# Optimization experiments

Hardware: AMD Instinct MI355X
Metric: run time of the kernel (lower is better)

Reference implementation:

```python
import jax, jax.numpy as jnp
import numpy as np

N_NODES = 50000
N_EDGES = 800000
N_FEAT = 256
HIDDEN = 128
N_CLASSES = 40


def gcn_conv(x, src, dst, W, b, n_nodes):
    """PyG GCNConv: add self-loops, symmetric normalization, x@W then scatter-add."""
    h = x @ W  # [N, out]
    loop = jnp.arange(n_nodes, dtype=src.dtype)
    s = jnp.concatenate([src, loop])  # [E+N]
    d = jnp.concatenate([dst, loop])
    deg = jax.ops.segment_sum(jnp.ones_like(d, dtype=h.dtype), d, num_segments=n_nodes)
    dinv = jnp.where(deg > 0, jax.lax.rsqrt(deg), 0.0)
    norm = dinv[s] * dinv[d]  # [E+N]
    msg = h[s] * norm[:, None]  # gather + scale
    out = jax.ops.segment_sum(msg, d, num_segments=n_nodes)  # scatter-add to targets
    return out + b


def setup_inputs() -> dict:
    key = jax.random.key(0)
    k1, k2, k3, k4 = jax.random.split(key, 4)
    x = jax.random.normal(k1, (N_NODES, N_FEAT), dtype=jnp.float32)
    edge_index = jax.random.randint(k2, (2, N_EDGES), 0, N_NODES, dtype=jnp.int32)
    # Glorot-style init for conv weights, zero bias (PyG default)
    W1 = jax.random.normal(k3, (N_FEAT, HIDDEN), dtype=jnp.float32) * (1.0 / np.sqrt(N_FEAT))
    b1 = jnp.zeros((HIDDEN,), dtype=jnp.float32)
    W2 = jax.random.normal(k4, (HIDDEN, N_CLASSES), dtype=jnp.float32) * (1.0 / np.sqrt(HIDDEN))
    b2 = jnp.zeros((N_CLASSES,), dtype=jnp.float32)
    return {"x": x, "edge_index": edge_index, "W1": W1, "b1": b1, "W2": W2, "b2": b2}


def reference(x, edge_index, W1, b1, W2, b2):
    # eval mode: dropout is identity
    src, dst = edge_index[0], edge_index[1]
    h = gcn_conv(x, src, dst, W1, b1, N_NODES)
    h = jax.nn.relu(h)
    h = gcn_conv(h, src, dst, W2, b2, N_NODES)
    return jax.nn.log_softmax(h, axis=1)
```

## Files before the change

kernel.cpp:

```cpp
#include <hip/hip_runtime.h>
#include <hip/hip_fp16.h>
#include <cstdint>

#define N_NODES 50000
#define N_EDGES 800000
#define N_FEAT 256
#define HIDDEN 128
#define N_CLASSES 40
#define NBUCKET 196
#define EPB 3125
#define BCAP 8192
#define ROWS_PAD 50048
#define G1_BLOCKS 782
#define H2S 64

typedef _Float16 half8 __attribute__((ext_vector_type(8)));
typedef __fp16 fp16x2 __attribute__((ext_vector_type(2)));
typedef __attribute__((ext_vector_type(4))) float f32x4;

__device__ inline ushort f2h(float f) {
    return __half_as_ushort(__float2half_rn(f));
}
__device__ inline __half2 u2h2(uint u) {
    union { uint u; __half2 h; } v; v.u = u; return v.h;
}
__device__ inline uint h22u(__half2 h) {
    union { __half2 h; uint u; } v; v.h = h; return v.u;
}


__global__ __launch_bounds__(256) void partition_repack(
        const int* __restrict__ src, const int* __restrict__ dst,
        int* __restrict__ cursor, uint* __restrict__ ebuf,
        const float* __restrict__ W1, ushort* __restrict__ Bp1,
        const float* __restrict__ W2, ushort* __restrict__ Bp2) {
    __shared__ int h[NBUCKET];
    __shared__ int base[NBUCKET];
    __shared__ int cur[NBUCKET];
    int blk = blockIdx.x, t = threadIdx.x;
    int gid = blk * 256 + t;
    if (gid < 32768) {
        int j = gid & 7, lane = (gid >> 3) & 63, kt = (gid >> 9) & 7, nt = gid >> 12;
        int k = kt * 32 + (lane >> 4) * 8 + j;
        int n = nt * 16 + (lane & 15);
        Bp1[gid] = f2h(W1[k * HIDDEN + n]);
    } else if (gid < 32768 + 6144) {
        int i2 = gid - 32768;
        int j = i2 & 7, lane = (i2 >> 3) & 63, kt = (i2 >> 9) & 3, nt = i2 >> 11;
        int k = kt * 32 + (lane >> 4) * 8 + j;
        int n = nt * 16 + (lane & 15);
        Bp2[i2] = (n < N_CLASSES) ? f2h(W2[k * N_CLASSES + n]) : (ushort)0;
    }
    if (t < NBUCKET) { h[t] = 0; cur[t] = 0; }
    __syncthreads();
    int eb = blk * EPB;
    for (int i = t; i < EPB; i += 256)
        atomicAdd(&h[dst[eb + i] >> 8], 1);
    __syncthreads();
    if (t < NBUCKET)
        base[t] = (h[t] > 0) ? atomicAdd(&cursor[t], h[t]) : 0;
    __syncthreads();
    for (int i = t; i < EPB; i += 256) {
        int d = dst[eb + i], sv = src[eb + i];
        int bk = d >> 8;
        int p = base[bk] + atomicAdd(&cur[bk], 1);
        ebuf[bk * BCAP + p] = ((uint)d << 16) | (uint)sv;
    }
}


__global__ __launch_bounds__(256) void csr_gemm1(
        const uint* __restrict__ ebuf, const int* __restrict__ cursor,
        int* __restrict__ deg, float* __restrict__ dinv,
        int* __restrict__ rowptr, int* __restrict__ esrc,
        const float* __restrict__ x, const ushort* __restrict__ Bp,
        ushort* __restrict__ h1h) {
    if (blockIdx.x < NBUCKET) {
        __shared__ int s[256];
        __shared__ int cnt[256];
        __shared__ int exc[256];
        __shared__ int cur[256];
        int b = blockIdx.x, t = threadIdx.x;
        s[t] = (t < NBUCKET) ? cursor[t] : 0;
        __syncthreads();
        for (int off = 1; off < 256; off <<= 1) {
            int t2 = 0;
            if (t >= off) t2 = s[t - off];
            __syncthreads();
            s[t] += t2;
            __syncthreads();
        }
        int beg = (b > 0) ? s[b - 1] : 0;
        int ecnt = s[b] - beg;
        __syncthreads();
        cnt[t] = 0;
        cur[t] = 0;
        __syncthreads();
        const uint* eb = ebuf + (size_t)b * BCAP;
        for (int i = t; i < ecnt; i += 256)
            atomicAdd(&cnt[(eb[i] >> 16) & 255], 1);
        __syncthreads();
        int d = cnt[t];
        s[t] = d;
        __syncthreads();
        for (int off = 1; off < 256; off <<= 1) {
            int t2 = 0;
            if (t >= off) t2 = s[t - off];
            __syncthreads();
            s[t] += t2;
            __syncthreads();
        }
        exc[t] = s[t] - d;
        int node = b * 256 + t;
        if (node < N_NODES) {
            deg[node] = d;
            dinv[node] = rsqrtf((float)(d + 1));
            rowptr[node] = beg + exc[t];
        }
        __syncthreads();
        for (int i = t; i < ecnt; i += 256) {
            uint u = eb[i];
            int dl = (int)(u >> 16) & 255;
            int pos = beg + exc[dl] + atomicAdd(&cur[dl], 1);
            esrc[pos] = (int)(u & 0xffffu);
        }
    } else {
        int t = threadIdx.x;
        int lane = t & 63, w = t >> 6;
        int r = lane & 15, q = lane >> 4;
        int row0 = (blockIdx.x - NBUCKET) * 64;
        int arow = row0 + w * 16 + r;
        if (arow >= N_NODES) arow = N_NODES - 1;
        const float* xrow = x + (size_t)arow * N_FEAT;
        f32x4 acc[8] = {};
        for (int kt = 0; kt < 8; ++kt) {
            float4 v0 = *(const float4*)(xrow + kt * 32 + q * 8);
            float4 v1 = *(const float4*)(xrow + kt * 32 + q * 8 + 4);
            union { fp16x2 p[4]; half8 a; } u;
            u.p[0] = __builtin_amdgcn_cvt_pkrtz(v0.x, v0.y);
            u.p[1] = __builtin_amdgcn_cvt_pkrtz(v0.z, v0.w);
            u.p[2] = __builtin_amdgcn_cvt_pkrtz(v1.x, v1.y);
            u.p[3] = __builtin_amdgcn_cvt_pkrtz(v1.z, v1.w);
#pragma unroll
            for (int nt = 0; nt < 8; ++nt) {
                half8 b = *(const half8*)(Bp + (((nt * 8 + kt) * 64) + lane) * 8);
                acc[nt] = __builtin_amdgcn_mfma_f32_16x16x32_f16(u.a, b, acc[nt], 0, 0, 0);
            }
        }
#pragma unroll
        for (int nt = 0; nt < 8; ++nt) {
            int col = nt * 16 + r;
#pragma unroll
            for (int reg = 0; reg < 4; ++reg) {
                int row = row0 + w * 16 + q * 4 + reg;
                if (row < N_NODES) h1h[(size_t)row * HIDDEN + col] = f2h(acc[nt][reg]);
            }
        }
    }
}


__global__ __launch_bounds__(256) void agg1_w2(
        const int* __restrict__ rowptr, const int* __restrict__ deg,
        const int* __restrict__ esrc, const float* __restrict__ dinv,
        const ushort* __restrict__ h1h, const float* __restrict__ b1,
        const ushort* __restrict__ Bp2, ushort* __restrict__ h2h) {
    int w = threadIdx.x >> 6, lane = threadIdx.x & 63;
    int v = blockIdx.x * 4 + w;
    int q = lane >> 4, l = lane & 15;
    int beg = rowptr[v], d = deg[v];
    float dv = dinv[v];
    __half2 z = __float2half2_rn(0.f);
    __half2 c0 = z, c1 = z, c2 = z, c3 = z;
    __half2 e0 = z, e1 = z, e2 = z, e3 = z;
    if (q == 0) {
        uint4 hv = *(const uint4*)(h1h + (size_t)v * HIDDEN + l * 8);
        __half2 gs = __float2half2_rn(dv * dv);
        c0 = __hfma2(u2h2(hv.x), gs, c0);
        c1 = __hfma2(u2h2(hv.y), gs, c1);
        c2 = __hfma2(u2h2(hv.z), gs, c2);
        c3 = __hfma2(u2h2(hv.w), gs, c3);
    }
    int e_l = (lane < d) ? esrc[beg + lane] : 0;
    float wd = (lane < d) ? dinv[e_l] * dv : 0.f;
    int whb = (int)h22u(__float2half2_rn(wd));
    int dm = min(d, 64);
    int i = 0;
    for (; i + 16 <= dm; i += 16) {
        int s0 = __shfl(e_l, i + q, 64);
        int s1 = __shfl(e_l, i + 4 + q, 64);
        int s2 = __shfl(e_l, i + 8 + q, 64);
        int s3 = __shfl(e_l, i + 12 + q, 64);
        __half2 gh0 = u2h2((uint)__shfl(whb, i + q, 64));
        __half2 gh1 = u2h2((uint)__shfl(whb, i + 4 + q, 64));
        __half2 gh2 = u2h2((uint)__shfl(whb, i + 8 + q, 64));
        __half2 gh3 = u2h2((uint)__shfl(whb, i + 12 + q, 64));
        uint4 h0 = *(const uint4*)(h1h + (size_t)s0 * HIDDEN + l * 8);
        uint4 h1 = *(const uint4*)(h1h + (size_t)s1 * HIDDEN + l * 8);
        uint4 h2 = *(const uint4*)(h1h + (size_t)s2 * HIDDEN + l * 8);
        uint4 h3 = *(const uint4*)(h1h + (size_t)s3 * HIDDEN + l * 8);
        c0 = __hfma2(u2h2(h0.x), gh0, c0);
        c1 = __hfma2(u2h2(h0.y), gh0, c1);
        c2 = __hfma2(u2h2(h0.z), gh0, c2);
        c3 = __hfma2(u2h2(h0.w), gh0, c3);
        e0 = __hfma2(u2h2(h1.x), gh1, e0);
        e1 = __hfma2(u2h2(h1.y), gh1, e1);
        e2 = __hfma2(u2h2(h1.z), gh1, e2);
        e3 = __hfma2(u2h2(h1.w), gh1, e3);
        c0 = __hfma2(u2h2(h2.x), gh2, c0);
        c1 = __hfma2(u2h2(h2.y), gh2, c1);
        c2 = __hfma2(u2h2(h2.z), gh2, c2);
        c3 = __hfma2(u2h2(h2.w), gh2, c3);
        e0 = __hfma2(u2h2(h3.x), gh3, e0);
        e1 = __hfma2(u2h2(h3.y), gh3, e1);
        e2 = __hfma2(u2h2(h3.z), gh3, e2);
        e3 = __hfma2(u2h2(h3.w), gh3, e3);
    }
    for (; i + 8 <= dm; i += 8) {
        int s0 = __shfl(e_l, i + q, 64);
        int s1 = __shfl(e_l, i + 4 + q, 64);
        __half2 gh0 = u2h2((uint)__shfl(whb, i + q, 64));
        __half2 gh1 = u2h2((uint)__shfl(whb, i + 4 + q, 64));
        uint4 h0 = *(const uint4*)(h1h + (size_t)s0 * HIDDEN + l * 8);
        uint4 h1 = *(const uint4*)(h1h + (size_t)s1 * HIDDEN + l * 8);
        c0 = __hfma2(u2h2(h0.x), gh0, c0);
        c1 = __hfma2(u2h2(h0.y), gh0, c1);
        c2 = __hfma2(u2h2(h0.z), gh0, c2);
        c3 = __hfma2(u2h2(h0.w), gh0, c3);
        e0 = __hfma2(u2h2(h1.x), gh1, e0);
        e1 = __hfma2(u2h2(h1.y), gh1, e1);
        e2 = __hfma2(u2h2(h1.z), gh1, e2);
        e3 = __hfma2(u2h2(h1.w), gh1, e3);
    }
    for (; i < dm; i += 4) {
        int idx = i + q;
        int cl = idx & 63;
        int s0 = __shfl(e_l, cl, 64);
        __half2 gh0 = u2h2((uint)__shfl(whb, cl, 64));
        if (idx >= dm) gh0 = z;
        uint4 h0 = *(const uint4*)(h1h + (size_t)s0 * HIDDEN + l * 8);
        c0 = __hfma2(u2h2(h0.x), gh0, c0);
        c1 = __hfma2(u2h2(h0.y), gh0, c1);
        c2 = __hfma2(u2h2(h0.z), gh0, c2);
        c3 = __hfma2(u2h2(h0.w), gh0, c3);
    }
    for (int j = 64 + q; j < d; j += 4) {
        int s = esrc[beg + j];
        __half2 g = __float2half2_rn(dinv[s] * dv);
        uint4 hs = *(const uint4*)(h1h + (size_t)s * HIDDEN + l * 8);
        c0 = __hfma2(u2h2(hs.x), g, c0);
        c1 = __hfma2(u2h2(hs.y), g, c1);
        c2 = __hfma2(u2h2(hs.z), g, c2);
        c3 = __hfma2(u2h2(hs.w), g, c3);
    }
    float2 f0 = __half22float2(c0), f1 = __half22float2(c1);
    float2 f2 = __half22float2(c2), f3 = __half22float2(c3);
    float2 g0 = __half22float2(e0), g1 = __half22float2(e1);
    float2 g2 = __half22float2(e2), g3 = __half22float2(e3);
    float a0 = f0.x + g0.x, a1 = f0.y + g0.y;
    float a2 = f1.x + g1.x, a3 = f1.y + g1.y;
    float a4 = f2.x + g2.x, a5 = f2.y + g2.y;
    float a6 = f3.x + g3.x, a7 = f3.y + g3.y;
    a0 += __shfl_xor(a0, 16, 64); a0 += __shfl_xor(a0, 32, 64);
    a1 += __shfl_xor(a1, 16, 64); a1 += __shfl_xor(a1, 32, 64);
    a2 += __shfl_xor(a2, 16, 64); a2 += __shfl_xor(a2, 32, 64);
    a3 += __shfl_xor(a3, 16, 64); a3 += __shfl_xor(a3, 32, 64);
    a4 += __shfl_xor(a4, 16, 64); a4 += __shfl_xor(a4, 32, 64);
    a5 += __shfl_xor(a5, 16, 64); a5 += __shfl_xor(a5, 32, 64);
    a6 += __shfl_xor(a6, 16, 64); a6 += __shfl_xor(a6, 32, 64);
    a7 += __shfl_xor(a7, 16, 64); a7 += __shfl_xor(a7, 32, 64);
    float4 bb0 = ((const float4*)b1)[l * 2];
    float4 bb1 = ((const float4*)b1)[l * 2 + 1];
    a0 += bb0.x; a1 += bb0.y; a2 += bb0.z; a3 += bb0.w;
    a4 += bb1.x; a5 += bb1.y; a6 += bb1.z; a7 += bb1.w;
    a0 = a0 > 0.f ? a0 : 0.f;  a1 = a1 > 0.f ? a1 : 0.f;
    a2 = a2 > 0.f ? a2 : 0.f;  a3 = a3 > 0.f ? a3 : 0.f;
    a4 = a4 > 0.f ? a4 : 0.f;  a5 = a5 > 0.f ? a5 : 0.f;
    a6 = a6 > 0.f ? a6 : 0.f;  a7 = a7 > 0.f ? a7 : 0.f;
    uint pk0 = ((uint)f2h(a1) << 16) | (uint)f2h(a0);
    uint pk1 = ((uint)f2h(a3) << 16) | (uint)f2h(a2);
    uint pk2 = ((uint)f2h(a5) << 16) | (uint)f2h(a4);
    uint pk3 = ((uint)f2h(a7) << 16) | (uint)f2h(a6);
    f32x4 acc[3] = {};
#pragma unroll
    for (int kt = 0; kt < 4; ++kt) {
        int srcl = kt * 4 + q;
        union { uint u[4]; half8 a; } ua;
        ua.u[0] = (uint)__shfl((int)pk0, srcl, 64);
        ua.u[1] = (uint)__shfl((int)pk1, srcl, 64);
        ua.u[2] = (uint)__shfl((int)pk2, srcl, 64);
        ua.u[3] = (uint)__shfl((int)pk3, srcl, 64);
#pragma unroll
        for (int nt = 0; nt < 3; ++nt) {
            half8 b = *(const half8*)(Bp2 + (((nt * 4 + kt) * 64) + lane) * 8);
            acc[nt] = __builtin_amdgcn_mfma_f32_16x16x32_f16(ua.a, b, acc[nt], 0, 0, 0);
        }
    }
    if (q == 0) {
        h2h[(size_t)v * H2S + l] = f2h(acc[0][0]);
    } else if (q == 1) {
        h2h[(size_t)v * H2S + 16 + l] = f2h(acc[1][0]);
    } else if (q == 2 && l < 8) {
        h2h[(size_t)v * H2S + 32 + l] = f2h(acc[2][0]);
    }
}


__global__ __launch_bounds__(256) void agg2_lsm(
        const int* __restrict__ rowptr, const int* __restrict__ deg,
        const int* __restrict__ esrc, const float* __restrict__ dinv,
        const ushort* __restrict__ h2h, const float* __restrict__ b2,
        float* __restrict__ out) {
    int t = threadIdx.x;
    int w = t >> 6, lane = t & 63;
    int half = lane >> 5, l = lane & 31;
    int v = blockIdx.x * 8 + w * 2 + half;
    int beg = rowptr[v], d = deg[v];
    float dv = dinv[v];
    __half2 z = __float2half2_rn(0.f);
    __half2 cA = z, cB = z;
    {
        uint hv = *(const uint*)(h2h + (size_t)v * H2S + l * 2);
        cA = __hfma2(u2h2(hv), __float2half2_rn(dv * dv), cA);
    }
    int e_l = (l < d) ? esrc[beg + l] : 0;
    float wd = (l < d) ? dinv[e_l] * dv : 0.f;
    int whb = (int)h22u(__float2half2_rn(wd));
    int dm = min(d, 32);
    int base = half * 32;
    int i = 0;
    for (; i + 8 <= dm; i += 8) {
        int s0 = __shfl(e_l, base + i + 0, 64);
        int s1 = __shfl(e_l, base + i + 1, 64);
        int s2 = __shfl(e_l, base + i + 2, 64);
        int s3 = __shfl(e_l, base + i + 3, 64);
        int s4 = __shfl(e_l, base + i + 4, 64);
        int s5 = __shfl(e_l, base + i + 5, 64);
        int s6 = __shfl(e_l, base + i + 6, 64);
        int s7 = __shfl(e_l, base + i + 7, 64);
        __half2 g0 = u2h2((uint)__shfl(whb, base + i + 0, 64));
        __half2 g1 = u2h2((uint)__shfl(whb, base + i + 1, 64));
        __half2 g2 = u2h2((uint)__shfl(whb, base + i + 2, 64));
        __half2 g3 = u2h2((uint)__shfl(whb, base + i + 3, 64));
        __half2 g4 = u2h2((uint)__shfl(whb, base + i + 4, 64));
        __half2 g5 = u2h2((uint)__shfl(whb, base + i + 5, 64));
        __half2 g6 = u2h2((uint)__shfl(whb, base + i + 6, 64));
        __half2 g7 = u2h2((uint)__shfl(whb, base + i + 7, 64));
        uint h0 = *(const uint*)(h2h + (size_t)s0 * H2S + l * 2);
        uint h1 = *(const uint*)(h2h + (size_t)s1 * H2S + l * 2);
        uint h2 = *(const uint*)(h2h + (size_t)s2 * H2S + l * 2);
        uint h3 = *(const uint*)(h2h + (size_t)s3 * H2S + l * 2);
        uint h4 = *(const uint*)(h2h + (size_t)s4 * H2S + l * 2);
        uint h5 = *(const uint*)(h2h + (size_t)s5 * H2S + l * 2);
        uint h6 = *(const uint*)(h2h + (size_t)s6 * H2S + l * 2);
        uint h7 = *(const uint*)(h2h + (size_t)s7 * H2S + l * 2);
        cA = __hfma2(u2h2(h0), g0, cA);
        cB = __hfma2(u2h2(h1), g1, cB);
        cA = __hfma2(u2h2(h2), g2, cA);
        cB = __hfma2(u2h2(h3), g3, cB);
        cA = __hfma2(u2h2(h4), g4, cA);
        cB = __hfma2(u2h2(h5), g5, cB);
        cA = __hfma2(u2h2(h6), g6, cA);
        cB = __hfma2(u2h2(h7), g7, cB);
    }
    for (; i + 4 <= dm; i += 4) {
        int s0 = __shfl(e_l, base + i + 0, 64);
        int s1 = __shfl(e_l, base + i + 1, 64);
        int s2 = __shfl(e_l, base + i + 2, 64);
        int s3 = __shfl(e_l, base + i + 3, 64);
        __half2 g0 = u2h2((uint)__shfl(whb, base + i + 0, 64));
        __half2 g1 = u2h2((uint)__shfl(whb, base + i + 1, 64));
        __half2 g2 = u2h2((uint)__shfl(whb, base + i + 2, 64));
        __half2 g3 = u2h2((uint)__shfl(whb, base + i + 3, 64));
        uint h0 = *(const uint*)(h2h + (size_t)s0 * H2S + l * 2);
        uint h1 = *(const uint*)(h2h + (size_t)s1 * H2S + l * 2);
        uint h2 = *(const uint*)(h2h + (size_t)s2 * H2S + l * 2);
        uint h3 = *(const uint*)(h2h + (size_t)s3 * H2S + l * 2);
        cA = __hfma2(u2h2(h0), g0, cA);
        cB = __hfma2(u2h2(h1), g1, cB);
        cA = __hfma2(u2h2(h2), g2, cA);
        cB = __hfma2(u2h2(h3), g3, cB);
    }
    for (; i < dm; ++i) {
        int s0 = __shfl(e_l, base + i, 64);
        __half2 g0 = u2h2((uint)__shfl(whb, base + i, 64));
        uint h0 = *(const uint*)(h2h + (size_t)s0 * H2S + l * 2);
        cA = __hfma2(u2h2(h0), g0, cA);
    }
    for (i = 32; i < d; ++i) {
        int s = esrc[beg + i];
        float g = dinv[s] * dv;
        uint hs = *(const uint*)(h2h + (size_t)s * H2S + l * 2);
        cA = __hfma2(u2h2(hs), __float2half2_rn(g), cA);
    }
    float2 fA = __half22float2(cA);
    float2 fB = __half22float2(cB);
    float ax = fA.x + fB.x, ay = fA.y + fB.y;
    if (l < 20) {
        float2 bb = ((const float2*)b2)[l];
        ax += bb.x; ay += bb.y;
    }
    float m = (l < 20) ? fmaxf(ax, ay) : -INFINITY;
#pragma unroll
    for (int off = 16; off; off >>= 1) m = fmaxf(m, __shfl_xor(m, off, 64));
    float e = (l < 20) ? (expf(ax - m) + expf(ay - m)) : 0.f;
#pragma unroll
    for (int off = 16; off; off >>= 1) e += __shfl_xor(e, off, 64);
    float ls = logf(e);
    if (l < 20) {
        float2 o;
        o.x = ax - m - ls;
        o.y = ay - m - ls;
        ((float2*)(out + (size_t)v * N_CLASSES))[l] = o;
    }
}


extern "C" void kernel_launch(void* const* d_in, const int* in_sizes, int n_in,
                              void* d_out, int out_size, void* d_ws, size_t ws_size,
                              hipStream_t stream) {
    const float* x  = (const float*)d_in[0];
    const int*   ei = (const int*)d_in[1];
    const float* W1 = (const float*)d_in[2];
    const float* b1 = (const float*)d_in[3];
    const float* W2 = (const float*)d_in[4];
    const float* b2 = (const float*)d_in[5];
    const int* src = ei;
    const int* dst = ei + N_EDGES;
    float* out = (float*)d_out;

    char* ws = (char*)d_ws;
    size_t off = 0;
    auto alloc = [&](size_t bytes) {
        void* p = ws + off;
        off += (bytes + 255) & ~(size_t)255;
        return p;
    };
    int*    cursor = (int*)alloc((size_t)NBUCKET * 4);
    int*    deg    = (int*)alloc((size_t)N_NODES * 4);
    float*  dinv   = (float*)alloc((size_t)N_NODES * 4);
    int*    rowptr = (int*)alloc((size_t)N_NODES * 4);
    uint*   ebuf   = (uint*)alloc((size_t)NBUCKET * BCAP * 4);
    int*    esrc   = (int*)alloc((size_t)N_EDGES * 4);
    ushort* Bp1    = (ushort*)alloc((size_t)32768 * 2);
    ushort* Bp2    = (ushort*)alloc((size_t)6144 * 2);
    ushort* h1h    = (ushort*)alloc((size_t)ROWS_PAD * HIDDEN * 2);
    ushort* h2h    = (ushort*)alloc((size_t)ROWS_PAD * H2S * 2);

    (void)hipMemsetAsync(cursor, 0, (size_t)NBUCKET * 4, stream);
    partition_repack<<<256, 256, 0, stream>>>(src, dst, cursor, ebuf, W1, Bp1, W2, Bp2);

    csr_gemm1<<<NBUCKET + G1_BLOCKS, 256, 0, stream>>>(
        ebuf, cursor, deg, dinv, rowptr, esrc, x, Bp1, h1h);

    agg1_w2<<<N_NODES / 4, 256, 0, stream>>>(rowptr, deg, esrc, dinv, h1h, b1, Bp2, h2h);

    agg2_lsm<<<N_NODES / 8, 256, 0, stream>>>(rowptr, deg, esrc, dinv, h2h, b2, out);
}
```

Baseline: 188.9 us.

## Pack source dinv into CSR edge words and shrink h2 row stride

Global in-degree counting moves into the partition kernel with atomics, so the CSR build can compute each source's dinv and pack it as fp16 beside the 16-bit source index in one 32-bit edge word. The aggregation kernels then no longer do a dependent random gather of dinv[src], and each edge needs a single shuffle instead of two. The h2 row stride drops from 64 to 40 halves, which cuts the footprint and cache lines touched by layer-2 gathers. The cost is 800k global atomics on deg and a larger memset, plus lower precision for the source normalization.

```diff
diff --git a/kernel.cpp b/kernel.cpp
--- a/kernel.cpp
+++ b/kernel.cpp
@@ -12,7 +12,7 @@
 #define BCAP 8192
 #define ROWS_PAD 50048
 #define G1_BLOCKS 782
-#define H2S 64
+#define H2S 40
 
 typedef _Float16 half8 __attribute__((ext_vector_type(8)));
 typedef __fp16 fp16x2 __attribute__((ext_vector_type(2)));
@@ -21,17 +21,22 @@
 __device__ inline ushort f2h(float f) {
     return __half_as_ushort(__float2half_rn(f));
 }
+__device__ inline float h2f_u(uint us) {
+    union { ushort u; __half h; } v; v.u = (ushort)us; return __half2float(v.h);
+}
 __device__ inline __half2 u2h2(uint u) {
     union { uint u; __half2 h; } v; v.u = u; return v.h;
 }
-__device__ inline uint h22u(__half2 h) {
-    union { __half2 h; uint u; } v; v.h = h; return v.u;
+
+__device__ inline uint wrep(uint u) {
+    uint t = u >> 16;
+    return (t << 16) | t;
 }
 
 
 __global__ __launch_bounds__(256) void partition_repack(
         const int* __restrict__ src, const int* __restrict__ dst,
-        int* __restrict__ cursor, uint* __restrict__ ebuf,
+        int* __restrict__ cursor, int* __restrict__ deg_g, uint* __restrict__ ebuf,
         const float* __restrict__ W1, ushort* __restrict__ Bp1,
         const float* __restrict__ W2, ushort* __restrict__ Bp2) {
     __shared__ int h[NBUCKET];
@@ -54,8 +59,11 @@
     if (t < NBUCKET) { h[t] = 0; cur[t] = 0; }
     __syncthreads();
     int eb = blk * EPB;
-    for (int i = t; i < EPB; i += 256)
-        atomicAdd(&h[dst[eb + i] >> 8], 1);
+    for (int i = t; i < EPB; i += 256) {
+        int d = dst[eb + i];
+        atomicAdd(&h[d >> 8], 1);
+        atomicAdd(&deg_g[d], 1);
+    }
     __syncthreads();
     if (t < NBUCKET)
         base[t] = (h[t] > 0) ? atomicAdd(&cursor[t], h[t]) : 0;
@@ -71,8 +79,8 @@
 
 __global__ __launch_bounds__(256) void csr_gemm1(
         const uint* __restrict__ ebuf, const int* __restrict__ cursor,
-        int* __restrict__ deg, float* __restrict__ dinv,
-        int* __restrict__ rowptr, int* __restrict__ esrc,
+        const int* __restrict__ deg_g, float* __restrict__ dinv,
+        int* __restrict__ rowptr, uint* __restrict__ esw,
         const float* __restrict__ x, const ushort* __restrict__ Bp,
         ushort* __restrict__ h1h) {
     if (blockIdx.x < NBUCKET) {
@@ -113,7 +121,6 @@
         exc[t] = s[t] - d;
         int node = b * 256 + t;
         if (node < N_NODES) {
-            deg[node] = d;
             dinv[node] = rsqrtf((float)(d + 1));
             rowptr[node] = beg + exc[t];
         }
@@ -121,8 +128,10 @@
         for (int i = t; i < ecnt; i += 256) {
             uint u = eb[i];
             int dl = (int)(u >> 16) & 255;
+            int sv = (int)(u & 0xffffu);
             int pos = beg + exc[dl] + atomicAdd(&cur[dl], 1);
-            esrc[pos] = (int)(u & 0xffffu);
+            float ds = rsqrtf((float)(deg_g[sv] + 1));
+            esw[pos] = (uint)sv | ((uint)f2h(ds) << 16);
         }
     } else {
         int t = threadIdx.x;
@@ -161,14 +170,14 @@
 
 
 __global__ __launch_bounds__(256) void agg1_w2(
-        const int* __restrict__ rowptr, const int* __restrict__ deg,
-        const int* __restrict__ esrc, const float* __restrict__ dinv,
+        const int* __restrict__ rowptr, const int* __restrict__ deg_g,
+        const uint* __restrict__ esw, const float* __restrict__ dinv,
         const ushort* __restrict__ h1h, const float* __restrict__ b1,
         const ushort* __restrict__ Bp2, ushort* __restrict__ h2h) {
     int w = threadIdx.x >> 6, lane = threadIdx.x & 63;
     int v = blockIdx.x * 4 + w;
     int q = lane >> 4, l = lane & 15;
-    int beg = rowptr[v], d = deg[v];
+    int beg = rowptr[v], d = deg_g[v];
     float dv = dinv[v];
     __half2 z = __float2half2_rn(0.f);
     __half2 c0 = z, c1 = z, c2 = z, c3 = z;
@@ -181,20 +190,21 @@
         c2 = __hfma2(u2h2(hv.z), gs, c2);
         c3 = __hfma2(u2h2(hv.w), gs, c3);
     }
-    int e_l = (lane < d) ? esrc[beg + lane] : 0;
-    float wd = (lane < d) ? dinv[e_l] * dv : 0.f;
-    int whb = (int)h22u(__float2half2_rn(wd));
+    uint u_own = (lane < d) ? esw[beg + lane] : 0u;
+    float wd = (lane < d) ? h2f_u(u_own >> 16) * dv : 0.f;
+    int up = (int)(((uint)f2h(wd) << 16) | (u_own & 0xffffu));
     int dm = min(d, 64);
     int i = 0;
     for (; i + 16 <= dm; i += 16) {
-        int s0 = __shfl(e_l, i + q, 64);
-        int s1 = __shfl(e_l, i + 4 + q, 64);
-        int s2 = __shfl(e_l, i + 8 + q, 64);
-        int s3 = __shfl(e_l, i + 12 + q, 64);
-        __half2 gh0 = u2h2((uint)__shfl(whb, i + q, 64));
-        __half2 gh1 = u2h2((uint)__shfl(whb, i + 4 + q, 64));
-        __half2 gh2 = u2h2((uint)__shfl(whb, i + 8 + q, 64));
-        __half2 gh3 = u2h2((uint)__shfl(whb, i + 12 + q, 64));
+        int u0 = __shfl(up, i + q, 64);
+        int u1 = __shfl(up, i + 4 + q, 64);
+        int u2 = __shfl(up, i + 8 + q, 64);
+        int u3 = __shfl(up, i + 12 + q, 64);
+        int s0 = u0 & 0xffff, s1 = u1 & 0xffff, s2 = u2 & 0xffff, s3 = u3 & 0xffff;
+        __half2 gh0 = u2h2(wrep((uint)u0));
+        __half2 gh1 = u2h2(wrep((uint)u1));
+        __half2 gh2 = u2h2(wrep((uint)u2));
+        __half2 gh3 = u2h2(wrep((uint)u3));
         uint4 h0 = *(const uint4*)(h1h + (size_t)s0 * HIDDEN + l * 8);
         uint4 h1 = *(const uint4*)(h1h + (size_t)s1 * HIDDEN + l * 8);
         uint4 h2 = *(const uint4*)(h1h + (size_t)s2 * HIDDEN + l * 8);
@@ -217,10 +227,11 @@
         e3 = __hfma2(u2h2(h3.w), gh3, e3);
     }
     for (; i + 8 <= dm; i += 8) {
-        int s0 = __shfl(e_l, i + q, 64);
-        int s1 = __shfl(e_l, i + 4 + q, 64);
-        __half2 gh0 = u2h2((uint)__shfl(whb, i + q, 64));
-        __half2 gh1 = u2h2((uint)__shfl(whb, i + 4 + q, 64));
+        int u0 = __shfl(up, i + q, 64);
+        int u1 = __shfl(up, i + 4 + q, 64);
+        int s0 = u0 & 0xffff, s1 = u1 & 0xffff;
+        __half2 gh0 = u2h2(wrep((uint)u0));
+        __half2 gh1 = u2h2(wrep((uint)u1));
         uint4 h0 = *(const uint4*)(h1h + (size_t)s0 * HIDDEN + l * 8);
         uint4 h1 = *(const uint4*)(h1h + (size_t)s1 * HIDDEN + l * 8);
         c0 = __hfma2(u2h2(h0.x), gh0, c0);
@@ -235,8 +246,9 @@
     for (; i < dm; i += 4) {
         int idx = i + q;
         int cl = idx & 63;
-        int s0 = __shfl(e_l, cl, 64);
-        __half2 gh0 = u2h2((uint)__shfl(whb, cl, 64));
+        int u0 = __shfl(up, cl, 64);
+        int s0 = u0 & 0xffff;
+        __half2 gh0 = u2h2(wrep((uint)u0));
         if (idx >= dm) gh0 = z;
         uint4 h0 = *(const uint4*)(h1h + (size_t)s0 * HIDDEN + l * 8);
         c0 = __hfma2(u2h2(h0.x), gh0, c0);
@@ -245,8 +257,9 @@
         c3 = __hfma2(u2h2(h0.w), gh0, c3);
     }
     for (int j = 64 + q; j < d; j += 4) {
-        int s = esrc[beg + j];
-        __half2 g = __float2half2_rn(dinv[s] * dv);
+        uint uu = esw[beg + j];
+        int s = (int)(uu & 0xffffu);
+        __half2 g = __float2half2_rn(h2f_u(uu >> 16) * dv);
         uint4 hs = *(const uint4*)(h1h + (size_t)s * HIDDEN + l * 8);
         c0 = __hfma2(u2h2(hs.x), g, c0);
         c1 = __hfma2(u2h2(hs.y), g, c1);
@@ -307,15 +320,15 @@
 
 
 __global__ __launch_bounds__(256) void agg2_lsm(
-        const int* __restrict__ rowptr, const int* __restrict__ deg,
-        const int* __restrict__ esrc, const float* __restrict__ dinv,
+        const int* __restrict__ rowptr, const int* __restrict__ deg_g,
+        const uint* __restrict__ esw, const float* __restrict__ dinv,
         const ushort* __restrict__ h2h, const float* __restrict__ b2,
         float* __restrict__ out) {
     int t = threadIdx.x;
     int w = t >> 6, lane = t & 63;
     int half = lane >> 5, l = lane & 31;
     int v = blockIdx.x * 8 + w * 2 + half;
-    int beg = rowptr[v], d = deg[v];
+    int beg = rowptr[v], d = deg_g[v];
     float dv = dinv[v];
     __half2 z = __float2half2_rn(0.f);
     __half2 cA = z, cB = z;
@@ -323,73 +336,61 @@
         uint hv = *(const uint*)(h2h + (size_t)v * H2S + l * 2);
         cA = __hfma2(u2h2(hv), __float2half2_rn(dv * dv), cA);
     }
-    int e_l = (l < d) ? esrc[beg + l] : 0;
-    float wd = (l < d) ? dinv[e_l] * dv : 0.f;
-    int whb = (int)h22u(__float2half2_rn(wd));
+    uint u_own = (l < d) ? esw[beg + l] : 0u;
+    float wd = (l < d) ? h2f_u(u_own >> 16) * dv : 0.f;
+    int up = (int)(((uint)f2h(wd) << 16) | (u_own & 0xffffu));
     int dm = min(d, 32);
     int base = half * 32;
     int i = 0;
     for (; i + 8 <= dm; i += 8) {
-        int s0 = __shfl(e_l, base + i + 0, 64);
-        int s1 = __shfl(e_l, base + i + 1, 64);
-        int s2 = __shfl(e_l, base + i + 2, 64);
-        int s3 = __shfl(e_l, base + i + 3, 64);
-        int s4 = __shfl(e_l, base + i + 4, 64);
-        int s5 = __shfl(e_l, base + i + 5, 64);
-        int s6 = __shfl(e_l, base + i + 6, 64);
-        int s7 = __shfl(e_l, base + i + 7, 64);
-        __half2 g0 = u2h2((uint)__shfl(whb, base + i + 0, 64));
-        __half2 g1 = u2h2((uint)__shfl(whb, base + i + 1, 64));
-        __half2 g2 = u2h2((uint)__shfl(whb, base + i + 2, 64));
-        __half2 g3 = u2h2((uint)__shfl(whb, base + i + 3, 64));
-        __half2 g4 = u2h2((uint)__shfl(whb, base + i + 4, 64));
-        __half2 g5 = u2h2((uint)__shfl(whb, base + i + 5, 64));
-        __half2 g6 = u2h2((uint)__shfl(whb, base + i + 6, 64));
-        __half2 g7 = u2h2((uint)__shfl(whb, base + i + 7, 64));
-        uint h0 = *(const uint*)(h2h + (size_t)s0 * H2S + l * 2);
-        uint h1 = *(const uint*)(h2h + (size_t)s1 * H2S + l * 2);
-        uint h2 = *(const uint*)(h2h + (size_t)s2 * H2S + l * 2);
-        uint h3 = *(const uint*)(h2h + (size_t)s3 * H2S + l * 2);
-        uint h4 = *(const uint*)(h2h + (size_t)s4 * H2S + l * 2);
-        uint h5 = *(const uint*)(h2h + (size_t)s5 * H2S + l * 2);
-        uint h6 = *(const uint*)(h2h + (size_t)s6 * H2S + l * 2);
-        uint h7 = *(const uint*)(h2h + (size_t)s7 * H2S + l * 2);
-        cA = __hfma2(u2h2(h0), g0, cA);
-        cB = __hfma2(u2h2(h1), g1, cB);
-        cA = __hfma2(u2h2(h2), g2, cA);
-        cB = __hfma2(u2h2(h3), g3, cB);
-        cA = __hfma2(u2h2(h4), g4, cA);
-        cB = __hfma2(u2h2(h5), g5, cB);
-        cA = __hfma2(u2h2(h6), g6, cA);
-        cB = __hfma2(u2h2(h7), g7, cB);
+        int u0 = __shfl(up, base + i + 0, 64);
+        int u1 = __shfl(up, base + i + 1, 64);
+        int u2 = __shfl(up, base + i + 2, 64);
+        int u3 = __shfl(up, base + i + 3, 64);
+        int u4 = __shfl(up, base + i + 4, 64);
+        int u5 = __shfl(up, base + i + 5, 64);
+        int u6 = __shfl(up, base + i + 6, 64);
+        int u7 = __shfl(up, base + i + 7, 64);
+        uint h0 = *(const uint*)(h2h + (size_t)(u0 & 0xffff) * H2S + l * 2);
+        uint h1 = *(const uint*)(h2h + (size_t)(u1 & 0xffff) * H2S + l * 2);
+        uint h2 = *(const uint*)(h2h + (size_t)(u2 & 0xffff) * H2S + l * 2);
+        uint h3 = *(const uint*)(h2h + (size_t)(u3 & 0xffff) * H2S + l * 2);
+        uint h4 = *(const uint*)(h2h + (size_t)(u4 & 0xffff) * H2S + l * 2);
+        uint h5 = *(const uint*)(h2h + (size_t)(u5 & 0xffff) * H2S + l * 2);
+        uint h6 = *(const uint*)(h2h + (size_t)(u6 & 0xffff) * H2S + l * 2);
+        uint h7 = *(const uint*)(h2h + (size_t)(u7 & 0xffff) * H2S + l * 2);
+        cA = __hfma2(u2h2(h0), u2h2(wrep((uint)u0)), cA);
+        cB = __hfma2(u2h2(h1), u2h2(wrep((uint)u1)), cB);
+        cA = __hfma2(u2h2(h2), u2h2(wrep((uint)u2)), cA);
+        cB = __hfma2(u2h2(h3), u2h2(wrep((uint)u3)), cB);
+        cA = __hfma2(u2h2(h4), u2h2(wrep((uint)u4)), cA);
+        cB = __hfma2(u2h2(h5), u2h2(wrep((uint)u5)), cB);
+        cA = __hfma2(u2h2(h6), u2h2(wrep((uint)u6)), cA);
+        cB = __hfma2(u2h2(h7), u2h2(wrep((uint)u7)), cB);
     }
     for (; i + 4 <= dm; i += 4) {
-        int s0 = __shfl(e_l, base + i + 0, 64);
-        int s1 = __shfl(e_l, base + i + 1, 64);
-        int s2 = __shfl(e_l, base + i + 2, 64);
-        int s3 = __shfl(e_l, base + i + 3, 64);
-        __half2 g0 = u2h2((uint)__shfl(whb, base + i + 0, 64));
-        __half2 g1 = u2h2((uint)__shfl(whb, base + i + 1, 64));
-        __half2 g2 = u2h2((uint)__shfl(whb, base + i + 2, 64));
-        __half2 g3 = u2h2((uint)__shfl(whb, base + i + 3, 64));
-        uint h0 = *(const uint*)(h2h + (size_t)s0 * H2S + l * 2);
-        uint h1 = *(const uint*)(h2h + (size_t)s1 * H2S + l * 2);
-        uint h2 = *(const uint*)(h2h + (size_t)s2 * H2S + l * 2);
-        uint h3 = *(const uint*)(h2h + (size_t)s3 * H2S + l * 2);
-        cA = __hfma2(u2h2(h0), g0, cA);
-        cB = __hfma2(u2h2(h1), g1, cB);
-        cA = __hfma2(u2h2(h2), g2, cA);
-        cB = __hfma2(u2h2(h3), g3, cB);
+        int u0 = __shfl(up, base + i + 0, 64);
+        int u1 = __shfl(up, base + i + 1, 64);
+        int u2 = __shfl(up, base + i + 2, 64);
+        int u3 = __shfl(up, base + i + 3, 64);
+        uint h0 = *(const uint*)(h2h + (size_t)(u0 & 0xffff) * H2S + l * 2);
+        uint h1 = *(const uint*)(h2h + (size_t)(u1 & 0xffff) * H2S + l * 2);
+        uint h2 = *(const uint*)(h2h + (size_t)(u2 & 0xffff) * H2S + l * 2);
+        uint h3 = *(const uint*)(h2h + (size_t)(u3 & 0xffff) * H2S + l * 2);
+        cA = __hfma2(u2h2(h0), u2h2(wrep((uint)u0)), cA);
+        cB = __hfma2(u2h2(h1), u2h2(wrep((uint)u1)), cB);
+        cA = __hfma2(u2h2(h2), u2h2(wrep((uint)u2)), cA);
+        cB = __hfma2(u2h2(h3), u2h2(wrep((uint)u3)), cB);
     }
     for (; i < dm; ++i) {
-        int s0 = __shfl(e_l, base + i, 64);
-        __half2 g0 = u2h2((uint)__shfl(whb, base + i, 64));
-        uint h0 = *(const uint*)(h2h + (size_t)s0 * H2S + l * 2);
-        cA = __hfma2(u2h2(h0), g0, cA);
+        int u0 = __shfl(up, base + i, 64);
+        uint h0 = *(const uint*)(h2h + (size_t)(u0 & 0xffff) * H2S + l * 2);
+        cA = __hfma2(u2h2(h0), u2h2(wrep((uint)u0)), cA);
     }
     for (i = 32; i < d; ++i) {
-        int s = esrc[beg + i];
-        float g = dinv[s] * dv;
+        uint uu = esw[beg + i];
+        int s = (int)(uu & 0xffffu);
+        float g = h2f_u(uu >> 16) * dv;
         uint hs = *(const uint*)(h2h + (size_t)s * H2S + l * 2);
         cA = __hfma2(u2h2(hs), __float2half2_rn(g), cA);
     }
@@ -436,24 +437,24 @@
         off += (bytes + 255) & ~(size_t)255;
         return p;
     };
-    int*    cursor = (int*)alloc((size_t)NBUCKET * 4);
-    int*    deg    = (int*)alloc((size_t)N_NODES * 4);
+    int*    cursor = (int*)alloc((size_t)(NBUCKET + N_NODES) * 4);
+    int*    deg_g  = cursor + NBUCKET;
     float*  dinv   = (float*)alloc((size_t)N_NODES * 4);
     int*    rowptr = (int*)alloc((size_t)N_NODES * 4);
     uint*   ebuf   = (uint*)alloc((size_t)NBUCKET * BCAP * 4);
-    int*    esrc   = (int*)alloc((size_t)N_EDGES * 4);
+    uint*   esw    = (uint*)alloc((size_t)N_EDGES * 4);
     ushort* Bp1    = (ushort*)alloc((size_t)32768 * 2);
     ushort* Bp2    = (ushort*)alloc((size_t)6144 * 2);
     ushort* h1h    = (ushort*)alloc((size_t)ROWS_PAD * HIDDEN * 2);
     ushort* h2h    = (ushort*)alloc((size_t)ROWS_PAD * H2S * 2);
 
-    (void)hipMemsetAsync(cursor, 0, (size_t)NBUCKET * 4, stream);
-    partition_repack<<<256, 256, 0, stream>>>(src, dst, cursor, ebuf, W1, Bp1, W2, Bp2);
+    (void)hipMemsetAsync(cursor, 0, (size_t)(NBUCKET + N_NODES) * 4, stream);
+    partition_repack<<<256, 256, 0, stream>>>(src, dst, cursor, deg_g, ebuf, W1, Bp1, W2, Bp2);
 
     csr_gemm1<<<NBUCKET + G1_BLOCKS, 256, 0, stream>>>(
-        ebuf, cursor, deg, dinv, rowptr, esrc, x, Bp1, h1h);
-
-    agg1_w2<<<N_NODES / 4, 256, 0, stream>>>(rowptr, deg, esrc, dinv, h1h, b1, Bp2, h2h);
-
-    agg2_lsm<<<N_NODES / 8, 256, 0, stream>>>(rowptr, deg, esrc, dinv, h2h, b2, out);
-}
+        ebuf, cursor, deg_g, dinv, rowptr, esw, x, Bp1, h1h);
+
+    agg1_w2<<<N_NODES / 4, 256, 0, stream>>>(rowptr, deg_g, esw, dinv, h1h, b1, Bp2, h2h);
+
+    agg2_lsm<<<N_NODES / 8, 256, 0, stream>>>(rowptr, deg_g, esw, dinv, h2h, b2, out);
+}
```

New measurement: 214.8 us. 13.7% more time.
